# Performance work log

Measured on AMD Instinct MI355X. Metric: run time of the kernel, lower is better.

The kernel has to match this reference:

```python
import jax, jax.numpy as jnp
import numpy as np

B, L, F, R = 8, 64, 64, 2048

def setup_inputs() -> dict:
    key = jax.random.key(0)
    k1, k2, k3, k4, k5, k6, k7 = jax.random.split(key, 7)
    return {
        "x": jax.random.normal(k1, (B, L, F, R), dtype=jnp.float32),
        "arg1_weight": jax.random.uniform(k2, (B, L), dtype=jnp.float32),
        "arg2_weight": jax.random.uniform(k3, (B, L), dtype=jnp.float32),
        "root_filler": jax.random.normal(k4, (B, F), dtype=jnp.float32),
        "cons_l": jax.random.normal(k5, (R, R), dtype=jnp.float32) / np.sqrt(R).astype(np.float32),
        "cons_r": jax.random.normal(k6, (R, R), dtype=jnp.float32) / np.sqrt(R).astype(np.float32),
        "root_role": jax.random.normal(k7, (R,), dtype=jnp.float32),
    }

def reference(x, arg1_weight, arg2_weight, root_filler, cons_l, cons_r, root_role):
    # Weighted reduction over memory slots: [B,L,F,R] x [B,L] -> [B,F,R]
    arg1 = jnp.einsum('blfr,bl->bfr', x, arg1_weight)
    arg2 = jnp.einsum('blfr,bl->bfr', x, arg2_weight)
    # F.linear on last (role) dim: y = arg @ W^T, plus root outer product
    output = (jnp.einsum('bfr,sr->bfs', arg1, cons_l)
              + jnp.einsum('bfr,sr->bfs', arg2, cons_r)
              + root_filler[:, :, None] * root_role[None, None, :])
    max1 = jnp.max(arg1_weight, axis=1)
    max2 = jnp.max(arg2_weight, axis=1)
    return (output, max1, max2)
```

## Files before the change

kernel.cpp:

```cpp
#include <hip/hip_runtime.h>
#include <stdint.h>

#define L_DIM 64
#define R_DIM 2048
#define M_DIM 512
#define K_DIM 4096
#define N_DIM 2048

typedef _Float16 half_t;
typedef _Float16 half4 __attribute__((ext_vector_type(4)));
typedef _Float16 half8 __attribute__((ext_vector_type(8)));
typedef float f4 __attribute__((ext_vector_type(4)));
typedef float floatx4 __attribute__((ext_vector_type(4)));

__global__ __launch_bounds__(512) void k_front(
    const float* __restrict__ x, const float* __restrict__ w1,
    const float* __restrict__ w2, half_t* __restrict__ Ah,
    float* __restrict__ out)
{
    const int tid = threadIdx.x;
    const int bid = blockIdx.x;

    if (bid < 512) {
        __shared__ float w1s[L_DIM], w2s[L_DIM];
        const int bf = bid;
        const int b  = bf >> 6;
        const int f  = bf & 63;
        if (tid < L_DIM) {
            w1s[tid] = w1[b * L_DIM + tid];
            w2s[tid] = w2[b * L_DIM + tid];
        }
        __syncthreads();
        const int r0 = tid * 4;
        const f4* xp = (const f4*)(x + ((size_t)(b * 4096 + f)) * 2048 + r0);
        float a1x=0.f,a1y=0.f,a1z=0.f,a1w=0.f;
        float a2x=0.f,a2y=0.f,a2z=0.f,a2w=0.f;
        #pragma unroll 8
        for (int l = 0; l < L_DIM; ++l) {
            f4 v = __builtin_nontemporal_load(xp + (size_t)l * (64 * R_DIM / 4));
            float u1 = w1s[l], u2 = w2s[l];
            a1x += v.x*u1; a1y += v.y*u1; a1z += v.z*u1; a1w += v.w*u1;
            a2x += v.x*u2; a2y += v.y*u2; a2z += v.z*u2; a2w += v.w*u2;
        }
        half4 h1 = { (half_t)a1x, (half_t)a1y, (half_t)a1z, (half_t)a1w };
        half4 h2 = { (half_t)a2x, (half_t)a2y, (half_t)a2z, (half_t)a2w };
        *(half4*)(Ah + (size_t)bf * K_DIM + r0) = h1;
        *(half4*)(Ah + (size_t)bf * K_DIM + R_DIM + r0) = h2;
    } else {
        if (tid < 16) {
            const float* src = (tid < 8) ? w1 : w2;
            const int b8 = tid & 7;
            float m = -1.f;
            #pragma unroll 8
            for (int l = 0; l < L_DIM; ++l)
                m = fmaxf(m, src[b8 * L_DIM + l]);
            out[(size_t)M_DIM * N_DIM + tid] = m;
        }
    }
}

__device__ __forceinline__ void gload16(void* lds, const void* g)
{
    __builtin_amdgcn_global_load_lds(
        (const __attribute__((address_space(1))) void*)g,
        (__attribute__((address_space(3))) void*)lds, 16, 0, 0);
}

#define BM 256
#define BN 128
#define BK 64
#define SPLITK 8
#define KSEG (K_DIM / SPLITK)
#define NSTEP (KSEG / BK)
#define SA_HALF (BM * BK)
#define SB_HALF (BN * BK)

__global__ __launch_bounds__(512) void k_gemm(
    const half_t* __restrict__ Ah, const float* __restrict__ cl,
    const float* __restrict__ cr, float* __restrict__ part)
{
    extern __shared__ half_t smem[];
    half_t* sA0 = smem;
    half_t* sB0 = smem + 2 * SA_HALF;

    const int tid  = threadIdx.x;
    const int lane = tid & 63;
    const int w    = tid >> 6;
    const int wr   = w >> 1, wc = w & 1;
    const int m0   = blockIdx.y * BM;
    const int n0   = blockIdx.x * BN;
    const int z    = blockIdx.z;
    const int kz   = z * KSEG;

    const int srow = lane >> 3;
    const int p8   = lane & 7;
    const int scol = (p8 ^ srow) << 3;
    const float* csrc = (z < 4) ? cl : cr;

    const floatx4 fzero = { 0.f, 0.f, 0.f, 0.f };
    floatx4 acc[4][4];
    #pragma unroll
    for (int i = 0; i < 4; ++i)
        #pragma unroll
        for (int j = 0; j < 4; ++j) acc[i][j] = fzero;

    auto stageA = [&](int buf, int kt) {
        half_t* sA = sA0 + buf * SA_HALF;
        #pragma unroll
        for (int c = 0; c < 4; ++c) {
            const int rbase = w * 32 + c * 8;
            const int row   = rbase + srow;
            gload16(&sA[rbase * BK], Ah + (size_t)(m0 + row) * K_DIM + kt + scol);
        }
    };
    auto loadB = [&](int kt, f4* regs) {
        const int ck = (kt & 2047) + scol;
        #pragma unroll
        for (int c = 0; c < 2; ++c) {
            const int row = w * 16 + c * 8 + srow;
            const float* src = csrc + (size_t)(n0 + row) * R_DIM + ck;
            regs[2 * c]     = *(const f4*)src;
            regs[2 * c + 1] = *(const f4*)(src + 4);
        }
    };
    auto writeB = [&](int buf, const f4* regs) {
        half_t* sB = sB0 + buf * SB_HALF;
        #pragma unroll
        for (int c = 0; c < 2; ++c) {
            const int row = w * 16 + c * 8 + srow;
            f4 lo = regs[2 * c], hi = regs[2 * c + 1];
            half8 h = { (half_t)lo.x, (half_t)lo.y, (half_t)lo.z, (half_t)lo.w,
                        (half_t)hi.x, (half_t)hi.y, (half_t)hi.z, (half_t)hi.w };
            *(half8*)&sB[row * BK + p8 * 8] = h;
        }
    };

    {
        f4 b0[4];
        loadB(kz, b0);
        stageA(0, kz);
        writeB(0, b0);
    }
    __syncthreads();

    const int l15 = lane & 15, l4 = lane >> 4;
    int buf = 0;
    for (int ks = 0; ks < NSTEP; ++ks) {
        f4 bn[4];
        const bool nxt = (ks + 1 < NSTEP);
        if (nxt) {
            loadB(kz + (ks + 1) * BK, bn);
            stageA(buf ^ 1, kz + (ks + 1) * BK);
        }
        half_t* sA = sA0 + buf * SA_HALF;
        half_t* sB = sB0 + buf * SB_HALF;
        #pragma unroll
        for (int ksub = 0; ksub < 2; ++ksub) {
            half8 af[4], bfr[4];
            const int cb = ksub * 4 + l4;
            #pragma unroll
            for (int mi = 0; mi < 4; ++mi) {
                const int row = wr * 64 + mi * 16 + l15;
                af[mi] = *(const half8*)&sA[row * BK + ((cb ^ (row & 7)) << 3)];
            }
            #pragma unroll
            for (int ni = 0; ni < 4; ++ni) {
                const int row = wc * 64 + ni * 16 + l15;
                bfr[ni] = *(const half8*)&sB[row * BK + ((cb ^ (row & 7)) << 3)];
            }
            #pragma unroll
            for (int mi = 0; mi < 4; ++mi)
                #pragma unroll
                for (int ni = 0; ni < 4; ++ni)
                    acc[mi][ni] = __builtin_amdgcn_mfma_f32_16x16x32_f16(
                        af[mi], bfr[ni], acc[mi][ni], 0, 0, 0);
        }
        if (nxt) writeB(buf ^ 1, bn);
        __syncthreads();
        buf ^= 1;
    }

    float* P = part + (size_t)z * ((size_t)M_DIM * N_DIM);
    #pragma unroll
    for (int mi = 0; mi < 4; ++mi) {
        const int rb = m0 + wr * 64 + mi * 16 + l4 * 4;
        #pragma unroll
        for (int ni = 0; ni < 4; ++ni) {
            const int cc = n0 + wc * 64 + ni * 16 + l15;
            #pragma unroll
            for (int r = 0; r < 4; ++r)
                P[(size_t)(rb + r) * N_DIM + cc] = acc[mi][ni][r];
        }
    }
}

__global__ __launch_bounds__(256) void k_final(
    const float* __restrict__ part, const float* __restrict__ filler,
    const float* __restrict__ role, float* __restrict__ out)
{
    const int idx = (blockIdx.x * 256 + threadIdx.x) * 4;
    const int mfi = idx >> 11;
    const int s   = idx & 2047;
    f4 a = *(const f4*)(part + idx);
    #pragma unroll
    for (int z = 1; z < SPLITK; ++z) {
        f4 p = *(const f4*)(part + (size_t)z * (M_DIM * (size_t)N_DIM) + idx);
        a.x += p.x; a.y += p.y; a.z += p.z; a.w += p.w;
    }
    const float fl = filler[mfi];
    f4 ro = *(const f4*)(role + s);
    a.x += fl * ro.x; a.y += fl * ro.y; a.z += fl * ro.z; a.w += fl * ro.w;
    *(f4*)(out + idx) = a;
}

extern "C" void kernel_launch(void* const* d_in, const int* in_sizes, int n_in,
                              void* d_out, int out_size, void* d_ws, size_t ws_size,
                              hipStream_t stream)
{
    const float* x      = (const float*)d_in[0];
    const float* w1     = (const float*)d_in[1];
    const float* w2     = (const float*)d_in[2];
    const float* filler = (const float*)d_in[3];
    const float* cl     = (const float*)d_in[4];
    const float* cr     = (const float*)d_in[5];
    const float* role   = (const float*)d_in[6];
    float* out = (float*)d_out;

    char* ws = (char*)d_ws;
    half_t* Ah  = (half_t*)ws;
    float*  prt = (float*)(ws + (4u << 20));

    const size_t lds_bytes = (2 * SA_HALF + 2 * SB_HALF) * sizeof(half_t);

    hipLaunchKernelGGL(k_front, dim3(513), dim3(512), 0, stream,
                       x, w1, w2, Ah, out);
    hipLaunchKernelGGL(k_gemm,  dim3(N_DIM / BN, M_DIM / BM, SPLITK), dim3(512),
                       lds_bytes, stream, Ah, cl, cr, prt);
    hipLaunchKernelGGL(k_final, dim3(1024), dim3(256), 0, stream, prt, filler, role, out);
}
```

Measured before the change: 73.60 us.

## Prefetch B two steps ahead in GEMM with manual waitcnts; widen front blocks

The GEMM main loop now keeps two register buffers for the B operand and loads B two k-steps ahead. It replaces __syncthreads with explicit s_waitcnt vmcnt/lgkmcnt counts and raw s_barrier, and fully unrolls the loop, so global latency for B and the async A loads overlaps more compute. The front reduction kernel uses 1024-thread blocks covering two f rows each, halving the block count. The hand-written waitcnt counts must match the exact number of outstanding loads, so if they are wrong the result is a race, and the extra registers may reduce occupancy.

Result: slower. 76.34 us (+3.7%).

```diff
diff --git a/kernel.cpp b/kernel.cpp
--- a/kernel.cpp
+++ b/kernel.cpp
@@ -13,7 +13,7 @@
 typedef float f4 __attribute__((ext_vector_type(4)));
 typedef float floatx4 __attribute__((ext_vector_type(4)));
 
-__global__ __launch_bounds__(512) void k_front(
+__global__ __launch_bounds__(1024) void k_front(
     const float* __restrict__ x, const float* __restrict__ w1,
     const float* __restrict__ w2, half_t* __restrict__ Ah,
     float* __restrict__ out)
@@ -21,18 +21,19 @@
     const int tid = threadIdx.x;
     const int bid = blockIdx.x;
 
-    if (bid < 512) {
+    if (bid < 256) {
         __shared__ float w1s[L_DIM], w2s[L_DIM];
-        const int bf = bid;
-        const int b  = bf >> 6;
-        const int f  = bf & 63;
+        const int b  = bid >> 5;
+        const int f0 = (bid & 31) * 2;
         if (tid < L_DIM) {
             w1s[tid] = w1[b * L_DIM + tid];
             w2s[tid] = w2[b * L_DIM + tid];
         }
         __syncthreads();
-        const int r0 = tid * 4;
-        const f4* xp = (const f4*)(x + ((size_t)(b * 4096 + f)) * 2048 + r0);
+        const int fo = tid >> 9;
+        const int r0 = (tid & 511) * 4;
+        const int bf = b * 64 + f0 + fo;
+        const f4* xp = (const f4*)(x + ((size_t)(b * 64) * 64 + f0 + fo) * 2048 + r0);
         float a1x=0.f,a1y=0.f,a1z=0.f,a1w=0.f;
         float a2x=0.f,a2y=0.f,a2z=0.f,a2w=0.f;
         #pragma unroll 8
@@ -135,25 +136,32 @@
         }
     };
 
-    {
-        f4 b0[4];
-        loadB(kz, b0);
-        stageA(0, kz);
-        writeB(0, b0);
-    }
-    __syncthreads();
+    f4 rB[2][4];
+
+    stageA(0, kz);
+    loadB(kz, rB[0]);
+    asm volatile("s_waitcnt vmcnt(0)" ::: "memory");
+    writeB(0, rB[0]);
+    loadB(kz + BK, rB[1]);
+    asm volatile("s_waitcnt lgkmcnt(0)" ::: "memory");
+    __builtin_amdgcn_s_barrier();
+    __builtin_amdgcn_sched_barrier(0);
 
     const int l15 = lane & 15, l4 = lane >> 4;
-    int buf = 0;
+    #pragma unroll
     for (int ks = 0; ks < NSTEP; ++ks) {
-        f4 bn[4];
-        const bool nxt = (ks + 1 < NSTEP);
-        if (nxt) {
-            loadB(kz + (ks + 1) * BK, bn);
-            stageA(buf ^ 1, kz + (ks + 1) * BK);
-        }
+        const int buf = ks & 1;
         half_t* sA = sA0 + buf * SA_HALF;
         half_t* sB = sB0 + buf * SB_HALF;
+        if (ks + 1 < NSTEP) stageA(buf ^ 1, kz + (ks + 1) * BK);
+        if (ks + 2 < NSTEP) loadB(kz + (ks + 2) * BK, rB[buf]);
+        if (ks + 1 < NSTEP) {
+            if (ks + 2 < NSTEP)
+                asm volatile("s_waitcnt vmcnt(8)" ::: "memory");
+            else
+                asm volatile("s_waitcnt vmcnt(4)" ::: "memory");
+            writeB(buf ^ 1, rB[(ks + 1) & 1]);
+        }
         #pragma unroll
         for (int ksub = 0; ksub < 2; ++ksub) {
             half8 af[4], bfr[4];
@@ -175,9 +183,14 @@
                     acc[mi][ni] = __builtin_amdgcn_mfma_f32_16x16x32_f16(
                         af[mi], bfr[ni], acc[mi][ni], 0, 0, 0);
         }
-        if (nxt) writeB(buf ^ 1, bn);
-        __syncthreads();
-        buf ^= 1;
+        if (ks + 1 < NSTEP) {
+            if (ks + 2 < NSTEP)
+                asm volatile("s_waitcnt vmcnt(4) lgkmcnt(0)" ::: "memory");
+            else
+                asm volatile("s_waitcnt vmcnt(0) lgkmcnt(0)" ::: "memory");
+            __builtin_amdgcn_s_barrier();
+            __builtin_amdgcn_sched_barrier(0);
+        }
     }
 
     float* P = part + (size_t)z * ((size_t)M_DIM * N_DIM);
@@ -232,7 +245,7 @@
 
     const size_t lds_bytes = (2 * SA_HALF + 2 * SB_HALF) * sizeof(half_t);
 
-    hipLaunchKernelGGL(k_front, dim3(513), dim3(512), 0, stream,
+    hipLaunchKernelGGL(k_front, dim3(257), dim3(1024), 0, stream,
                        x, w1, w2, Ah, out);
     hipLaunchKernelGGL(k_gemm,  dim3(N_DIM / BN, M_DIM / BM, SPLITK), dim3(512),
                        lds_bytes, stream, Ah, cl, cr, prt);
```
